# Optimization experiments

Hardware: AMD Instinct MI355X
Metric: run time of the kernel (lower is better)

Reference implementation:

```python
import jax, jax.numpy as jnp
import numpy as np

B, C_IN, C_OUT = 4, 64, 64
Z = H = W = 64
MZ = MH = MW = 16
R = 16


def setup_inputs() -> dict:
    key = jax.random.key(0)
    ks = jax.random.split(key, 12)
    p = lambda k, s: jax.random.normal(k, s, jnp.float32) * 0.02
    return {
        "x": jax.random.normal(ks[0], (B, C_IN, Z, H, W), jnp.float32),
        "U_in": p(ks[1], (C_IN, R)),
        "U_out": p(ks[2], (C_OUT, R)),
        "U_z": p(ks[3], (MZ, R)),
        "U_h": p(ks[4], (MH, R)),
        "U_w": p(ks[5], (MW, R)),
        "U_z2": p(ks[6], (MZ, R)),
        "U_h2": p(ks[7], (MH, R)),
        "core_r": p(ks[8], (R, R, R, R, R)),
        "core_i": p(ks[9], (R, R, R, R, R)),
        "core2_r": p(ks[10], (R, R, R, R, R)),
        "core2_i": p(ks[11], (R, R, R, R, R)),
    }


def _reconstruct(U_in, U_out, Uz, Uh, Uw, core):
    # Original: einsum('ir,or,zr,hr,wr,abcde->iozwh', ..., core).
    # core's a..e indices are summed independently of the shared r index,
    # so the weight equals the CP outer product scaled by core.sum().
    c = jnp.complex64
    w = jnp.einsum('ir,or,zr,hr,wr->iozwh',
                   U_in.astype(c), U_out.astype(c), Uz.astype(c),
                   Uh.astype(c), Uw.astype(c))
    return w * jnp.sum(core)  # (in, out, mz, mw, mh)


def reference(x, U_in, U_out, U_z, U_h, U_w, U_z2, U_h2,
              core_r, core_i, core2_r, core2_i):
    mz, mh, mw = U_z.shape[0], U_h.shape[0], U_w.shape[0]
    b, _, z, h, w = x.shape
    core = core_r + 1j * core_i
    core2 = core2_r + 1j * core2_i

    x_ft = jnp.fft.rfftn(x, axes=(-3, -2, -1))  # (B, Cin, Z, H, W//2+1) c64
    w1 = _reconstruct(U_in, U_out, U_z, U_h, U_w, core)
    w2 = _reconstruct(U_in, U_out, U_z2, U_h2, U_w, core2)

    lo = jnp.einsum('bixyz,ioxyz->boxyz', x_ft[:, :, :mz, :mh, :mw], w1)
    hi = jnp.einsum('bixyz,ioxyz->boxyz', x_ft[:, :, -mz:, :mh, :mw], w2)

    out_ft = jnp.zeros((b, U_out.shape[0], z, h, w // 2 + 1), jnp.complex64)
    out_ft = out_ft.at[:, :, :mz, :mh, :mw].set(lo)
    out_ft = out_ft.at[:, :, -mz:, :mh, :mw].set(hi)

    return jnp.fft.irfftn(out_ft, s=(z, h, w), axes=(-3, -2, -1)).astype(jnp.float32)
```

## Files before the change

### kernel.cpp

```cpp
#include <hip/hip_runtime.h>

#define TWOPI 6.28318530717958647692f

constexpr float COSQ[17] = {
  1.0f, 0.995184727f, 0.980785280f, 0.956940336f, 0.923879533f,
  0.881921264f, 0.831469612f, 0.773010453f, 0.707106781f,
  0.634393284f, 0.555570233f, 0.471396737f, 0.382683432f,
  0.290284677f, 0.195090322f, 0.098017140f, 0.0f
};
__host__ __device__ constexpr float cos64f(int k) {
  k &= 63;
  return (k <= 16) ? COSQ[k] : (k < 32) ? -COSQ[32 - k]
       : (k <= 48) ? -COSQ[k - 32] : COSQ[64 - k];
}
__host__ __device__ constexpr float sin64f(int k) { return cos64f(k + 48); }


__global__ __launch_bounds__(256) void k_fwd_wh_core(
    const float* __restrict__ x, float2* __restrict__ A2,
    const float* __restrict__ a0, const float* __restrict__ a1,
    const float* __restrict__ a2, const float* __restrict__ a3,
    float* __restrict__ partial) {
  __shared__ float2 T[4][64][17];
  __shared__ float red[256];
  if (blockIdx.x < 256) {
    int bx = blockIdx.x & 63, by = blockIdx.x >> 6;
    const float* p = by == 0 ? a0 : by == 1 ? a1 : by == 2 ? a2 : a3;
    const float4* p4 = (const float4*)p;
    float s = 0.f;
    int base = bx * 4096 + threadIdx.x;
    #pragma unroll
    for (int i = 0; i < 16; ++i) {
      float4 v = p4[base + i * 256];
      s += (v.x + v.y) + (v.z + v.w);
    }
    red[threadIdx.x] = s;
    __syncthreads();
    for (int off = 128; off; off >>= 1) {
      if (threadIdx.x < off) red[threadIdx.x] += red[threadIdx.x + off];
      __syncthreads();
    }
    if (threadIdx.x == 0) partial[by * 64 + bx] = red[0];
    return;
  }
  int wave = threadIdx.x >> 6, lane = threadIdx.x & 63;
  int plane = (blockIdx.x - 256) * 4 + wave;
  const float* xp = x + (size_t)plane * 4096 + lane;
  float cre[16], cim[16];
  {
    float x0 = xp[0], x32 = xp[32 * 64];
    #pragma unroll
    for (int hf = 0; hf < 16; ++hf) {
      cre[hf] = x0 + ((hf & 1) ? -x32 : x32);
      cim[hf] = 0.f;
    }
  }
  #pragma unroll
  for (int h = 1; h < 32; ++h) {
    float va = xp[h * 64], vb = xp[(64 - h) * 64];
    float u = va + vb, d = va - vb;
    #pragma unroll
    for (int hf = 0; hf < 16; ++hf) {
      cre[hf] = fmaf(u, cos64f(h * hf), cre[hf]);
      cim[hf] = fmaf(d, -sin64f(h * hf), cim[hf]);
    }
  }
  #pragma unroll
  for (int hf = 0; hf < 16; ++hf)
    T[wave][lane][hf] = make_float2(cre[hf], cim[hf]);
  __syncthreads();
  int hf = lane & 15, wq = lane >> 4;
  float2 rot[4], CS[4], acc[4];
  float2 T0 = T[wave][0][hf], T32 = T[wave][32][hf];
  #pragma unroll
  for (int j = 0; j < 4; ++j) {
    int wf = wq + 4 * j;
    float s, c;
    sincosf((TWOPI / 64.f) * (float)wf, &s, &c);
    rot[j] = make_float2(c, s);
    CS[j] = make_float2(c, s);
    float sgn = (wf & 1) ? -1.f : 1.f;
    acc[j] = make_float2(T0.x + sgn * T32.x, T0.y + sgn * T32.y);
  }
  #pragma unroll 4
  for (int w = 1; w < 32; ++w) {
    float2 a = T[wave][w][hf], b2 = T[wave][64 - w][hf];
    float Sr = a.x + b2.x, Si = a.y + b2.y;
    float Dr = a.x - b2.x, Di = a.y - b2.y;
    #pragma unroll
    for (int j = 0; j < 4; ++j) {
      float C = CS[j].x, Sn = CS[j].y;
      acc[j].x = fmaf(Sr, C, fmaf(Di, Sn, acc[j].x));
      acc[j].y = fmaf(Si, C, fmaf(-Dr, Sn, acc[j].y));
      float nC = C * rot[j].x - Sn * rot[j].y;
      CS[j].y = fmaf(C, rot[j].y, Sn * rot[j].x);
      CS[j].x = nC;
    }
  }
  float2* dst = A2 + (size_t)plane * 256 + lane;
  #pragma unroll
  for (int j = 0; j < 4; ++j) dst[j * 64] = acc[j];
}

__global__ __launch_bounds__(256) void k_proj(const float2* __restrict__ A2,
                                              float2* __restrict__ P,
                                              const float* __restrict__ U_in,
                                              const float* __restrict__ partial,
                                              float* __restrict__ S) {
  if (blockIdx.x == 0 && blockIdx.y == 0 && threadIdx.x < 4) {
    float s = 0.f;
    for (int j = 0; j < 64; ++j) s += partial[threadIdx.x * 64 + j];
    S[threadIdx.x] = s;
  }
  __shared__ float sU[1024];
  int t = threadIdx.x;
  #pragma unroll
  for (int i = 0; i < 4; ++i) sU[t + 256 * i] = U_in[t + 256 * i];
  __syncthreads();
  int b = blockIdx.x >> 6, z = blockIdx.x & 63, r0 = blockIdx.y * 8;
  const float2* src = A2 + (((size_t)b * 64) * 64 + z) * 256 + t;
  float2 acc[8];
  #pragma unroll
  for (int r = 0; r < 8; ++r) acc[r] = make_float2(0.f, 0.f);
  for (int c = 0; c < 64; ++c) {
    float2 v = src[(size_t)c * 16384];
    #pragma unroll
    for (int r = 0; r < 8; ++r) {
      float u = sU[c * 16 + r0 + r];
      acc[r].x = fmaf(v.x, u, acc[r].x);
      acc[r].y = fmaf(v.y, u, acc[r].y);
    }
  }
  float2* dst = P + (((size_t)b * 16 + r0) * 64 + z) * 256 + t;
  #pragma unroll
  for (int r = 0; r < 8; ++r) dst[(size_t)r * 16384] = acc[r];
}

template <int Y>
__device__ __forceinline__ void inv_z_q(const float* __restrict__ gr,
                                        const float* __restrict__ gi,
                                        float2* __restrict__ dst) {
  if (Y == 0) {
    float sr = 0.f, si = 0.f;
    #pragma unroll
    for (int k = 0; k < 32; ++k) { sr += gr[k]; si += gi[k]; }
    dst[0] = make_float2(sr, si);
  }
  if (Y == 2) {
    float sr = 0.f, si = 0.f;
    #pragma unroll
    for (int k = 0; k < 32; ++k) {
      if (k & 1) { sr -= gr[k]; si -= gi[k]; }
      else       { sr += gr[k]; si += gi[k]; }
    }
    dst[32 * 256] = make_float2(sr, si);
  }
  constexpr int z0 = (Y == 0) ? 1 : (Y == 1) ? 9 : (Y == 2) ? 17 : 25;
  constexpr int z1 = (Y == 0) ? 8 : (Y == 1) ? 16 : (Y == 2) ? 24 : 31;
  #pragma unroll
  for (int z = z0; z <= z1; ++z) {
    float Ar = 0.f, Ai = 0.f, Br = 0.f, Bi = 0.f;
    #pragma unroll
    for (int k = 0; k < 32; ++k) {
      const int f = (k < 16) ? k : (k + 32);
      const float c = cos64f(z * f), s = sin64f(z * f);
      Ar = fmaf(gr[k], c, Ar); Ai = fmaf(gi[k], c, Ai);
      Br = fmaf(gr[k], s, Br); Bi = fmaf(gi[k], s, Bi);
    }
    dst[z * 256] = make_float2(Ar - Bi, Ai + Br);
    dst[(64 - z) * 256] = make_float2(Ar + Bi, Ai - Br);
  }
}

__global__ __launch_bounds__(256) void k_zmix(
    const float2* __restrict__ P, float2* __restrict__ Q,
    const float* __restrict__ U_z, const float* __restrict__ U_h,
    const float* __restrict__ U_w, const float* __restrict__ U_z2,
    const float* __restrict__ U_h2, const float* __restrict__ S4) {
  int br = blockIdx.x, r = br & 15, t = threadIdx.x;
  int hf = t & 15, wf = ((t >> 4) & 3) + 4 * (t >> 6);
  const float2* src = P + (size_t)br * 16384 + t;
  float2 acc[32];
  {
    float2 v0 = src[0], v32 = src[32 * 256];
    #pragma unroll
    for (int k = 0; k < 16; ++k) {
      float sgn = (k & 1) ? -1.f : 1.f;
      float2 e = make_float2(v0.x + sgn * v32.x, v0.y + sgn * v32.y);
      acc[k] = e;
      acc[k + 16] = e;
    }
  }
  #pragma unroll
  for (int z = 1; z < 32; ++z) {
    float2 a = src[z * 256], b = src[(64 - z) * 256];
    float Sr = a.x + b.x, Si = a.y + b.y;
    float Dr = a.x - b.x, Di = a.y - b.y;
    #pragma unroll
    for (int k = 0; k < 16; ++k) {
      {
        const float c = cos64f(z * k), s = sin64f(z * k);
        acc[k].x = fmaf(Sr, c, fmaf(Di, s, acc[k].x));
        acc[k].y = fmaf(Si, c, fmaf(-Dr, s, acc[k].y));
      }
      {
        const float c = cos64f(z * (k + 48)), s = sin64f(z * (k + 48));
        acc[k + 16].x = fmaf(Sr, c, fmaf(Di, s, acc[k + 16].x));
        acc[k + 16].y = fmaf(Si, c, fmaf(-Dr, s, acc[k + 16].y));
      }
    }
  }
  const float invN = 1.0f / 262144.0f;
  float S1r = S4[0] * invN, S1i = S4[1] * invN;
  float S2r = S4[2] * invN, S2i = S4[3] * invN;
  float cw = U_w[hf * 16 + r];
  float ch1 = U_h[wf * 16 + r] * cw, ch2 = U_h2[wf * 16 + r] * cw;
  float gr[32], gi[32];
  #pragma unroll
  for (int k = 0; k < 16; ++k) {
    float2 v = acc[k];
    float g = U_z[k * 16 + r] * ch1;
    float Fr = S1r * g, Fi = S1i * g;
    gr[k] = v.x * Fr - v.y * Fi;
    gi[k] = v.x * Fi + v.y * Fr;
  }
  #pragma unroll
  for (int k = 0; k < 16; ++k) {
    float2 v = acc[k + 16];
    float g = U_z2[k * 16 + r] * ch2;
    float Fr = S2r * g, Fi = S2i * g;
    gr[k + 16] = v.x * Fr - v.y * Fi;
    gi[k + 16] = v.x * Fi + v.y * Fr;
  }
  float2* dst = Q + (size_t)br * 16384 + t;
  switch (blockIdx.y) {
    case 0: inv_z_q<0>(gr, gi, dst); break;
    case 1: inv_z_q<1>(gr, gi, dst); break;
    case 2: inv_z_q<2>(gr, gi, dst); break;
    default: inv_z_q<3>(gr, gi, dst); break;
  }
}

__global__ __launch_bounds__(256) void k_inv_hw_ex(
    const float2* __restrict__ Q, float* __restrict__ out,
    const float* __restrict__ U_out) {
  __shared__ float2 sQ[16][256];
  __shared__ float2 GLo[4][256];
  __shared__ float sU[1024];
  int t = threadIdx.x;
  int b = blockIdx.x >> 6, z = blockIdx.x & 63, og = blockIdx.y;
  #pragma unroll
  for (int i = 0; i < 4; ++i) sU[t + 256 * i] = U_out[t + 256 * i];
  #pragma unroll
  for (int r = 0; r < 16; ++r)
    sQ[r][t] = Q[((size_t)(b * 16 + r) * 64 + z) * 256 + t];
  __syncthreads();
  int wave = t >> 6, lane = t & 63;
  float2 E2[16];
  {
    float s, c;
    sincosf((TWOPI / 64.f) * (float)lane, &s, &c);
    float2 E = make_float2(c, s);
    float2 St = E;
    #pragma unroll
    for (int wfi = 1; wfi < 16; ++wfi) {
      E2[wfi] = make_float2(E.x + E.x, E.y + E.y);
      float ex = E.x * St.x - E.y * St.y;
      E.y = fmaf(E.x, St.y, E.y * St.x);
      E.x = ex;
    }
  }
  for (int oi = 0; oi < 4; ++oi) {
    int o = og * 16 + wave * 4 + oi;
    #pragma unroll
    for (int q = 0; q < 4; ++q) {
      int tt = lane + 64 * q;
      float re = 0.f, im = 0.f;
      #pragma unroll
      for (int r = 0; r < 16; ++r) {
        float u = sU[o * 16 + r];
        float2 v = sQ[r][tt];
        re = fmaf(v.x, u, re);
        im = fmaf(v.y, u, im);
      }
      GLo[wave][tt] = make_float2(re, im);
    }
    float qre[16], qim[16];
    #pragma unroll
    for (int hfi = 0; hfi < 16; ++hfi) {
      float2 g0 = GLo[wave][hfi];
      float ar = g0.x, ai = g0.y;
      #pragma unroll
      for (int wfi = 1; wfi < 16; ++wfi) {
        float2 gv = GLo[wave][(wfi >> 2) * 64 + (wfi & 3) * 16 + hfi];
        ar = fmaf(gv.x, E2[wfi].x, fmaf(-gv.y, E2[wfi].y, ar));
        ai = fmaf(gv.x, E2[wfi].y, fmaf(gv.y, E2[wfi].x, ai));
      }
      qre[hfi] = ar; qim[hfi] = ai;
    }
    float* op = out + (((size_t)(b * 64 + o) * 64 + z)) * 4096 + lane;
    {
      float Pv = qre[0];
      #pragma unroll
      for (int hfi = 1; hfi < 16; ++hfi) Pv += qre[hfi];
      op[0] = Pv;
    }
    {
      float Pv = qre[0];
      #pragma unroll
      for (int hfi = 1; hfi < 16; ++hfi)
        Pv += (hfi & 1) ? -qre[hfi] : qre[hfi];
      op[32 * 64] = Pv;
    }
    #pragma unroll
    for (int h = 1; h < 32; ++h) {
      float Pv = qre[0], Qv = 0.f;
      #pragma unroll
      for (int hfi = 1; hfi < 16; ++hfi) {
        Pv = fmaf(qre[hfi], cos64f(h * hfi), Pv);
        Qv = fmaf(qim[hfi], sin64f(h * hfi), Qv);
      }
      op[h * 64] = Pv - Qv;
      op[(64 - h) * 64] = Pv + Qv;
    }
  }
}

extern "C" void kernel_launch(void* const* d_in, const int* in_sizes, int n_in,
                              void* d_out, int out_size, void* d_ws,
                              size_t ws_size, hipStream_t stream) {
  const float* x    = (const float*)d_in[0];
  const float* Uin  = (const float*)d_in[1];
  const float* Uout = (const float*)d_in[2];
  const float* Uz   = (const float*)d_in[3];
  const float* Uh   = (const float*)d_in[4];
  const float* Uw   = (const float*)d_in[5];
  const float* Uz2  = (const float*)d_in[6];
  const float* Uh2  = (const float*)d_in[7];
  const float* cr   = (const float*)d_in[8];
  const float* ci   = (const float*)d_in[9];
  const float* c2r  = (const float*)d_in[10];
  const float* c2i  = (const float*)d_in[11];
  float* outp = (float*)d_out;

  char* ws = (char*)d_ws;
  float* S       = (float*)ws;
  float* partial = (float*)(ws + 256);
  float2* A2 = (float2*)(ws + 4096);
  float2* P  = (float2*)(ws + 33558528);
  float2* Q  = (float2*)(ws + 41947136);

  k_fwd_wh_core<<<4352, 256, 0, stream>>>(x, A2, cr, ci, c2r, c2i, partial);
  k_proj<<<dim3(256, 2), 256, 0, stream>>>(A2, P, Uin, partial, S);
  k_zmix<<<dim3(64, 4), 256, 0, stream>>>(P, Q, Uz, Uh, Uw, Uz2, Uh2, S);
  k_inv_hw_ex<<<dim3(256, 4), 256, 0, stream>>>(Q, outp, Uout);
}
```

Baseline: 191.0 us.

## Fuse forward W/H DFT with U_in channel projection to drop A2 intermediate

Merges the forward H/W DFT kernel and the channel projection kernel into one. Each block now loops over all 64 input channels for one (batch, z) slice and accumulates the rank-16 projection in registers via shared memory, so the large A2 buffer is never written to or read back from global memory. The core-sum reduction moves into k_zmix, which removes one kernel launch. The trade-off is far fewer compute blocks (256 instead of 4096), each running a serial 16-iteration loop with extra barriers, which lowers occupancy and the ability to hide memory latency.

Result: slower. 223.6 us (+17.1%).

```diff
diff --git a/kernel.cpp b/kernel.cpp
--- a/kernel.cpp
+++ b/kernel.cpp
@@ -16,124 +16,129 @@
 __host__ __device__ constexpr float sin64f(int k) { return cos64f(k + 48); }
 
 
-__global__ __launch_bounds__(256) void k_fwd_wh_core(
-    const float* __restrict__ x, float2* __restrict__ A2,
+__global__ __launch_bounds__(256) void k_fwd_proj_core(
+    const float* __restrict__ x, float2* __restrict__ P,
+    const float* __restrict__ U_in,
     const float* __restrict__ a0, const float* __restrict__ a1,
     const float* __restrict__ a2, const float* __restrict__ a3,
     float* __restrict__ partial) {
   __shared__ float2 T[4][64][17];
+  __shared__ float2 A4[4][256];
+  __shared__ float sU[1024];
   __shared__ float red[256];
+  int t = threadIdx.x;
   if (blockIdx.x < 256) {
     int bx = blockIdx.x & 63, by = blockIdx.x >> 6;
     const float* p = by == 0 ? a0 : by == 1 ? a1 : by == 2 ? a2 : a3;
     const float4* p4 = (const float4*)p;
     float s = 0.f;
-    int base = bx * 4096 + threadIdx.x;
+    int base = bx * 4096 + t;
     #pragma unroll
     for (int i = 0; i < 16; ++i) {
       float4 v = p4[base + i * 256];
       s += (v.x + v.y) + (v.z + v.w);
     }
-    red[threadIdx.x] = s;
+    red[t] = s;
     __syncthreads();
     for (int off = 128; off; off >>= 1) {
-      if (threadIdx.x < off) red[threadIdx.x] += red[threadIdx.x + off];
+      if (t < off) red[t] += red[t + off];
       __syncthreads();
     }
-    if (threadIdx.x == 0) partial[by * 64 + bx] = red[0];
+    if (t == 0) partial[by * 64 + bx] = red[0];
     return;
   }
-  int wave = threadIdx.x >> 6, lane = threadIdx.x & 63;
-  int plane = (blockIdx.x - 256) * 4 + wave;
-  const float* xp = x + (size_t)plane * 4096 + lane;
-  float cre[16], cim[16];
-  {
-    float x0 = xp[0], x32 = xp[32 * 64];
-    #pragma unroll
-    for (int hf = 0; hf < 16; ++hf) {
-      cre[hf] = x0 + ((hf & 1) ? -x32 : x32);
-      cim[hf] = 0.f;
-    }
-  }
-  #pragma unroll
-  for (int h = 1; h < 32; ++h) {
-    float va = xp[h * 64], vb = xp[(64 - h) * 64];
-    float u = va + vb, d = va - vb;
-    #pragma unroll
-    for (int hf = 0; hf < 16; ++hf) {
-      cre[hf] = fmaf(u, cos64f(h * hf), cre[hf]);
-      cim[hf] = fmaf(d, -sin64f(h * hf), cim[hf]);
-    }
-  }
-  #pragma unroll
-  for (int hf = 0; hf < 16; ++hf)
-    T[wave][lane][hf] = make_float2(cre[hf], cim[hf]);
+  int wave = t >> 6, lane = t & 63;
+  int b = (blockIdx.x - 256) >> 6, z = (blockIdx.x - 256) & 63;
+  #pragma unroll
+  for (int i = 0; i < 4; ++i) sU[t + 256 * i] = U_in[t + 256 * i];
+  int hf2 = lane & 15, wq = lane >> 4;
+  float2 rot[4], CS0[4];
+  #pragma unroll
+  for (int j = 0; j < 4; ++j) {
+    float s, c;
+    sincosf((TWOPI / 64.f) * (float)(wq + 4 * j), &s, &c);
+    rot[j] = make_float2(c, s);
+    CS0[j] = make_float2(c, s);
+  }
+  float2 pacc[4][4];
+  #pragma unroll
+  for (int r = 0; r < 4; ++r)
+    #pragma unroll
+    for (int j = 0; j < 4; ++j) pacc[r][j] = make_float2(0.f, 0.f);
   __syncthreads();
-  int hf = lane & 15, wq = lane >> 4;
-  float2 rot[4], CS[4], acc[4];
-  float2 T0 = T[wave][0][hf], T32 = T[wave][32][hf];
-  #pragma unroll
-  for (int j = 0; j < 4; ++j) {
-    int wf = wq + 4 * j;
-    float s, c;
-    sincosf((TWOPI / 64.f) * (float)wf, &s, &c);
-    rot[j] = make_float2(c, s);
-    CS[j] = make_float2(c, s);
-    float sgn = (wf & 1) ? -1.f : 1.f;
-    acc[j] = make_float2(T0.x + sgn * T32.x, T0.y + sgn * T32.y);
-  }
-  #pragma unroll 4
-  for (int w = 1; w < 32; ++w) {
-    float2 a = T[wave][w][hf], b2 = T[wave][64 - w][hf];
-    float Sr = a.x + b2.x, Si = a.y + b2.y;
-    float Dr = a.x - b2.x, Di = a.y - b2.y;
+  for (int ri = 0; ri < 16; ++ri) {
+    int c = ri * 4 + wave;
+    const float* xp = x + (((size_t)(b * 64 + c) * 64 + z)) * 4096 + lane;
+    float cre[16], cim[16];
+    {
+      float x0 = xp[0], x32 = xp[32 * 64];
+      #pragma unroll
+      for (int hf = 0; hf < 16; ++hf) {
+        cre[hf] = x0 + ((hf & 1) ? -x32 : x32);
+        cim[hf] = 0.f;
+      }
+    }
+    #pragma unroll
+    for (int h = 1; h < 32; ++h) {
+      float va = xp[h * 64], vb = xp[(64 - h) * 64];
+      float u = va + vb, d = va - vb;
+      #pragma unroll
+      for (int hf = 0; hf < 16; ++hf) {
+        cre[hf] = fmaf(u, cos64f(h * hf), cre[hf]);
+        cim[hf] = fmaf(d, -sin64f(h * hf), cim[hf]);
+      }
+    }
+    #pragma unroll
+    for (int hf = 0; hf < 16; ++hf)
+      T[wave][lane][hf] = make_float2(cre[hf], cim[hf]);
+    float2 CS[4], acc[4];
+    float2 T0 = T[wave][0][hf2], T32 = T[wave][32][hf2];
     #pragma unroll
     for (int j = 0; j < 4; ++j) {
-      float C = CS[j].x, Sn = CS[j].y;
-      acc[j].x = fmaf(Sr, C, fmaf(Di, Sn, acc[j].x));
-      acc[j].y = fmaf(Si, C, fmaf(-Dr, Sn, acc[j].y));
-      float nC = C * rot[j].x - Sn * rot[j].y;
-      CS[j].y = fmaf(C, rot[j].y, Sn * rot[j].x);
-      CS[j].x = nC;
-    }
-  }
-  float2* dst = A2 + (size_t)plane * 256 + lane;
-  #pragma unroll
-  for (int j = 0; j < 4; ++j) dst[j * 64] = acc[j];
-}
-
-__global__ __launch_bounds__(256) void k_proj(const float2* __restrict__ A2,
-                                              float2* __restrict__ P,
-                                              const float* __restrict__ U_in,
-                                              const float* __restrict__ partial,
-                                              float* __restrict__ S) {
-  if (blockIdx.x == 0 && blockIdx.y == 0 && threadIdx.x < 4) {
-    float s = 0.f;
-    for (int j = 0; j < 64; ++j) s += partial[threadIdx.x * 64 + j];
-    S[threadIdx.x] = s;
-  }
-  __shared__ float sU[1024];
-  int t = threadIdx.x;
-  #pragma unroll
-  for (int i = 0; i < 4; ++i) sU[t + 256 * i] = U_in[t + 256 * i];
-  __syncthreads();
-  int b = blockIdx.x >> 6, z = blockIdx.x & 63, r0 = blockIdx.y * 8;
-  const float2* src = A2 + (((size_t)b * 64) * 64 + z) * 256 + t;
-  float2 acc[8];
-  #pragma unroll
-  for (int r = 0; r < 8; ++r) acc[r] = make_float2(0.f, 0.f);
-  for (int c = 0; c < 64; ++c) {
-    float2 v = src[(size_t)c * 16384];
-    #pragma unroll
-    for (int r = 0; r < 8; ++r) {
-      float u = sU[c * 16 + r0 + r];
-      acc[r].x = fmaf(v.x, u, acc[r].x);
-      acc[r].y = fmaf(v.y, u, acc[r].y);
-    }
-  }
-  float2* dst = P + (((size_t)b * 16 + r0) * 64 + z) * 256 + t;
-  #pragma unroll
-  for (int r = 0; r < 8; ++r) dst[(size_t)r * 16384] = acc[r];
+      CS[j] = CS0[j];
+      float sgn = ((wq + 4 * j) & 1) ? -1.f : 1.f;
+      acc[j] = make_float2(T0.x + sgn * T32.x, T0.y + sgn * T32.y);
+    }
+    #pragma unroll 4
+    for (int w = 1; w < 32; ++w) {
+      float2 a = T[wave][w][hf2], b2 = T[wave][64 - w][hf2];
+      float Sr = a.x + b2.x, Si = a.y + b2.y;
+      float Dr = a.x - b2.x, Di = a.y - b2.y;
+      #pragma unroll
+      for (int j = 0; j < 4; ++j) {
+        float C = CS[j].x, Sn = CS[j].y;
+        acc[j].x = fmaf(Sr, C, fmaf(Di, Sn, acc[j].x));
+        acc[j].y = fmaf(Si, C, fmaf(-Dr, Sn, acc[j].y));
+        float nC = C * rot[j].x - Sn * rot[j].y;
+        CS[j].y = fmaf(C, rot[j].y, Sn * rot[j].x);
+        CS[j].x = nC;
+      }
+    }
+    #pragma unroll
+    for (int j = 0; j < 4; ++j) A4[wave][j * 64 + lane] = acc[j];
+    __syncthreads();
+    #pragma unroll
+    for (int cc = 0; cc < 4; ++cc) {
+      #pragma unroll
+      for (int j = 0; j < 4; ++j) {
+        float2 v = A4[cc][j * 64 + lane];
+        #pragma unroll
+        for (int r = 0; r < 4; ++r) {
+          float u = sU[(ri * 4 + cc) * 16 + wave * 4 + r];
+          pacc[r][j].x = fmaf(v.x, u, pacc[r][j].x);
+          pacc[r][j].y = fmaf(v.y, u, pacc[r][j].y);
+        }
+      }
+    }
+    __syncthreads();
+  }
+  #pragma unroll
+  for (int r = 0; r < 4; ++r) {
+    float2* dst =
+        P + (((size_t)(b * 16 + wave * 4 + r) * 64 + z)) * 256 + lane;
+    #pragma unroll
+    for (int j = 0; j < 4; ++j) dst[j * 64] = pacc[r][j];
+  }
 }
 
 template <int Y>
@@ -176,8 +181,14 @@
     const float2* __restrict__ P, float2* __restrict__ Q,
     const float* __restrict__ U_z, const float* __restrict__ U_h,
     const float* __restrict__ U_w, const float* __restrict__ U_z2,
-    const float* __restrict__ U_h2, const float* __restrict__ S4) {
+    const float* __restrict__ U_h2, const float* __restrict__ partial) {
+  __shared__ float sS[4];
   int br = blockIdx.x, r = br & 15, t = threadIdx.x;
+  if (t < 4) {
+    float s = 0.f;
+    for (int j = 0; j < 64; ++j) s += partial[t * 64 + j];
+    sS[t] = s;
+  }
   int hf = t & 15, wf = ((t >> 4) & 3) + 4 * (t >> 6);
   const float2* src = P + (size_t)br * 16384 + t;
   float2 acc[32];
@@ -210,9 +221,10 @@
       }
     }
   }
+  __syncthreads();
   const float invN = 1.0f / 262144.0f;
-  float S1r = S4[0] * invN, S1i = S4[1] * invN;
-  float S2r = S4[2] * invN, S2i = S4[3] * invN;
+  float S1r = sS[0] * invN, S1i = sS[1] * invN;
+  float S2r = sS[2] * invN, S2i = sS[3] * invN;
   float cw = U_w[hf * 16 + r];
   float ch1 = U_h[wf * 16 + r] * cw, ch2 = U_h2[wf * 16 + r] * cw;
   float gr[32], gi[32];
@@ -344,14 +356,13 @@
   float* outp = (float*)d_out;
 
   char* ws = (char*)d_ws;
-  float* S       = (float*)ws;
   float* partial = (float*)(ws + 256);
-  float2* A2 = (float2*)(ws + 4096);
-  float2* P  = (float2*)(ws + 33558528);
-  float2* Q  = (float2*)(ws + 41947136);
-
-  k_fwd_wh_core<<<4352, 256, 0, stream>>>(x, A2, cr, ci, c2r, c2i, partial);
-  k_proj<<<dim3(256, 2), 256, 0, stream>>>(A2, P, Uin, partial, S);
-  k_zmix<<<dim3(64, 4), 256, 0, stream>>>(P, Q, Uz, Uh, Uw, Uz2, Uh2, S);
+  float2* P  = (float2*)(ws + 4096);
+  float2* Q  = (float2*)(ws + 4096 + 8388608);
+
+  k_fwd_proj_core<<<512, 256, 0, stream>>>(x, P, Uin, cr, ci, c2r, c2i,
+                                           partial);
+  k_zmix<<<dim3(64, 4), 256, 0, stream>>>(P, Q, Uz, Uh, Uw, Uz2, Uh2,
+                                          partial);
   k_inv_hw_ex<<<dim3(256, 4), 256, 0, stream>>>(Q, outp, Uout);
 }
```
